# Kernel tuning notes

Measured on AMD Instinct MI355X. Metric: run time of the kernel, lower is better.

## Reference

```python
import jax, jax.numpy as jnp
import numpy as np

B, H, T, IN_DIM, OUT_DIM = 4096, 256, 128, 7, 3

def _u(key, shape, fan_in):
    s = 1.0 / np.sqrt(fan_in)
    return jax.random.uniform(key, shape, jnp.float32, -s, s)

def setup_inputs() -> dict:
    key = jax.random.key(0)
    ks = jax.random.split(key, 12)
    return {
        "metadata": jax.random.normal(ks[0], (B, IN_DIM), jnp.float32),
        "target_seq_len": T,
        # encoder_fc: Linear(7, H) -> ReLU -> Linear(H, 2H) -> ReLU
        "W1": _u(ks[1], (H, IN_DIM), IN_DIM), "b1": _u(ks[2], (H,), IN_DIM),
        "W2": _u(ks[3], (2 * H, H), H),       "b2": _u(ks[4], (2 * H,), H),
        # decoder LSTM (single layer, torch gate order i,f,g,o)
        "Wih": _u(ks[5], (4 * H, OUT_DIM), H), "Whh": _u(ks[6], (4 * H, H), H),
        "bih": _u(ks[7], (4 * H,), H),         "bhh": _u(ks[8], (4 * H,), H),
        # fc_out: Linear(H, H//2) -> ReLU -> Linear(H//2, 3)
        "Wo1": _u(ks[9], (H // 2, H), H),      "bo1": _u(ks[10], (H // 2,), H),
        "Wo2": _u(ks[11], (OUT_DIM, H // 2), H // 2),
        "bo2": jnp.zeros((OUT_DIM,), jnp.float32),
    }

def reference(metadata, target_seq_len, W1, b1, W2, b2,
              Wih, Whh, bih, bhh, Wo1, bo1, Wo2, bo2):
    hid = Whh.shape[1]
    # encoder MLP -> [B, 2H]; split into initial (h0, c0)
    enc = jax.nn.relu(metadata @ W1.T + b1)
    enc = jax.nn.relu(enc @ W2.T + b2)
    h0, c0 = enc[:, :hid], enc[:, hid:]
    x0 = metadata[:, :3]  # first decoder input = start position

    def step(carry, _):
        h, c, x = carry
        gates = x @ Wih.T + bih + h @ Whh.T + bhh  # [B, 4H]
        i, f, g, o = jnp.split(gates, 4, axis=-1)
        c = jax.nn.sigmoid(f) * c + jax.nn.sigmoid(i) * jnp.tanh(g)
        h = jax.nn.sigmoid(o) * jnp.tanh(c)
        y = jax.nn.relu(h @ Wo1.T + bo1) @ Wo2.T + bo2  # [B, 3]
        return (h, c, y), y

    _, ys = jax.lax.scan(step, (h0, c0, x0), None, length=target_seq_len)
    return jnp.transpose(ys, (1, 0, 2))  # [B, T, 3]
```

## Files before the change

### kernel.cpp

```cpp
#include <hip/hip_runtime.h>

typedef __bf16 bf16_t;
typedef bf16_t bf16x8 __attribute__((ext_vector_type(8)));
typedef float  f32x4  __attribute__((ext_vector_type(4)));

#define MFMA16(A, B, C) __builtin_amdgcn_mfma_f32_16x16x32_bf16((A), (B), (C), 0, 0, 0)

static constexpr int KEXT   = 288;
static constexpr int HS     = 296;
static constexpr int GS     = 264;
static constexpr int TSTEPS = 128;
static constexpr int TILE_B = 16;

static constexpr int WALL_OFF = 0;
static constexpr int W2E_OFF  = 1152 * 288;
static constexpr int WO2E_OFF = W2E_OFF + 512 * 288;
static constexpr int WS_ELEMS = WO2E_OFF + 16 * 128;

__global__ __launch_bounds__(256) void prep_kernel(
    const float* __restrict__ W2,  const float* __restrict__ b2,
    const float* __restrict__ Wih, const float* __restrict__ Whh,
    const float* __restrict__ bih, const float* __restrict__ bhh,
    const float* __restrict__ Wo1, const float* __restrict__ bo1,
    const float* __restrict__ Wo2, bf16_t* __restrict__ ws)
{
    int idx = blockIdx.x * 256 + threadIdx.x;
    if (idx < 1152 * 288) {
        int r = idx / 288, k = idx - r * 288;
        float v = 0.f;
        if (r < 1024) {
            if (k < 256)       v = Whh[r * 256 + k];
            else if (k < 259)  v = Wih[r * 3 + (k - 256)];
            else if (k == 259) v = bih[r] + bhh[r];
        } else {
            int q = r - 1024;
            if (k < 256)       v = Wo1[q * 256 + k];
            else if (k == 259) v = bo1[q];
        }
        ws[WALL_OFF + idx] = (bf16_t)v;
    } else if (idx < W2E_OFF + 512 * 288) {
        int j = idx - W2E_OFF;
        int u = j / 288, k = j - u * 288;
        float v = 0.f;
        if (k < 256)       v = W2[u * 256 + k];
        else if (k == 259) v = b2[u];
        ws[idx] = (bf16_t)v;
    } else if (idx < WS_ELEMS) {
        int j = idx - WO2E_OFF;
        int d = j >> 7, q = j & 127;
        ws[idx] = (bf16_t)((d < 3) ? Wo2[d * 128 + q] : 0.f);
    }
}

__device__ __forceinline__ float rcp_f(float x) {
    float r; asm("v_rcp_f32 %0, %1" : "=v"(r) : "v"(x)); return r;
}
__device__ __forceinline__ float sigm(float x) { return rcp_f(1.f + __expf(-x)); }
__device__ __forceinline__ float tanh_f(float x) {
    float e = __expf(2.f * x);
    return 1.f - 2.f * rcp_f(e + 1.f);
}
__device__ __forceinline__ unsigned pk2(float a, float b) {
    union { bf16_t h[2]; unsigned u; } x;
    x.h[0] = (bf16_t)a; x.h[1] = (bf16_t)b; return x.u;
}

__device__ __forceinline__ void bar_lds() {
    asm volatile("s_waitcnt lgkmcnt(0)" ::: "memory");
    __builtin_amdgcn_s_barrier();
}

__global__ __launch_bounds__(512, 2) void lstm_main(
    const float* __restrict__ meta, const float* __restrict__ W1,
    const float* __restrict__ b1,   const float* __restrict__ bo2,
    const bf16_t* __restrict__ ws,  float* __restrict__ out)
{
    __shared__ __align__(16) bf16_t hx[2][TILE_B][HS];
    __shared__ __align__(16) bf16_t wg[256][GS];
    __shared__ __align__(16) bf16_t wo2l[16][136];
    __shared__ __align__(16) bf16_t zbuf[TILE_B][136];

    const int tid  = threadIdx.x;
    const int wv   = tid >> 6;
    const int lane = tid & 63;
    const int l15  = lane & 15;
    const int quad = lane >> 4;
    const int gb   = blockIdx.x * TILE_B;

    const bf16_t* wall = ws + WALL_OFF;
    const bf16_t* w2e  = ws + W2E_OFF;
    const bf16_t* wo2e = ws + WO2E_OFF;
    const f32x4 zero4 = {0.f, 0.f, 0.f, 0.f};

    if (tid < 32) {
        int buf = tid >> 4, b = tid & 15;
        for (int c2 = 256; c2 < HS; ++c2)
            hx[buf][b][c2] = (bf16_t)((c2 == 259) ? 1.f : 0.f);
    }
    {
        int b = tid & 15, j0 = (tid >> 4) * 8;
        float m[7];
        #pragma unroll
        for (int k = 0; k < 7; ++k) m[k] = meta[(size_t)(gb + b) * 7 + k];
        #pragma unroll
        for (int jj = 0; jj < 8; ++jj) {
            int jd = j0 + jj;
            float acc = b1[jd];
            #pragma unroll
            for (int k = 0; k < 7; ++k) acc += W1[jd * 7 + k] * m[k];
            hx[1][b][jd] = (bf16_t)fmaxf(acc, 0.f);
        }
    }
    __syncthreads();

    float* cbuf = (float*)&wg[0][0];
    {
        f32x4 e[4] = {zero4, zero4, zero4, zero4};
        #pragma unroll
        for (int kk = 0; kk < 9; ++kk) {
            int ko = 32 * kk + 8 * quad;
            bf16x8 bf = *(const bf16x8*)&hx[1][l15][ko];
            #pragma unroll
            for (int m = 0; m < 4; ++m) {
                bf16x8 aa = *(const bf16x8*)&w2e[(size_t)(64 * wv + 16 * m + l15) * KEXT + ko];
                e[m] = MFMA16(aa, bf, e[m]);
            }
        }
        #pragma unroll
        for (int m = 0; m < 4; ++m) {
            int row = 64 * wv + 16 * m + 4 * quad;
            if (row < 256) {
                *(unsigned*)&hx[0][l15][row]     = pk2(fmaxf(e[m][0], 0.f), fmaxf(e[m][1], 0.f));
                *(unsigned*)&hx[0][l15][row + 2] = pk2(fmaxf(e[m][2], 0.f), fmaxf(e[m][3], 0.f));
            } else {
                int d = row - 256;
                #pragma unroll
                for (int r = 0; r < 4; ++r)
                    cbuf[(size_t)(d + r) * 17 + l15] = fmaxf(e[m][r], 0.f);
            }
        }
    }
    __syncthreads();

    f32x4 c[2];
    #pragma unroll
    for (int half = 0; half < 2; ++half)
        #pragma unroll
        for (int r = 0; r < 4; ++r)
            c[half][r] = cbuf[(size_t)(32 * wv + 16 * half + 4 * quad + r) * 17 + l15];
    __syncthreads();

    #pragma unroll
    for (int i = 0; i < 17; ++i) {
        int idx = tid + 512 * i;
        if (idx < 256 * 33) {
            int r = idx / 33, c8 = idx - r * 33;
            *(bf16x8*)&wg[r][8 * c8] = *(const bf16x8*)&wall[(size_t)(512 + r) * KEXT + 8 * c8];
        }
    }
    #pragma unroll
    for (int i = 0; i < 4; ++i) {
        int idx = tid + 512 * i;
        int r = idx >> 7, cc = idx & 127;
        wo2l[r][cc] = wo2e[r * 128 + cc];
    }

    bf16x8 af[2][2][9];
    #pragma unroll
    for (int g = 0; g < 2; ++g)
        #pragma unroll
        for (int h = 0; h < 2; ++h)
            #pragma unroll
            for (int kk = 0; kk < 9; ++kk)
                af[g][h][kk] = *(const bf16x8*)&wall[(size_t)(256 * g + 32 * wv + 16 * h + l15) * KEXT
                                                     + 32 * kk + 8 * quad];

    const bf16_t* obase = wall + (size_t)(768  + 32 * wv + l15) * KEXT + 8 * quad;
    const bf16_t* wbase = wall + (size_t)(1024 + 16 * wv + l15) * KEXT + 8 * quad;

    const float bo2v0 = bo2[0], bo2v1 = bo2[1], bo2v2 = bo2[2];

    bf16x8 ob[3][2];
    #pragma unroll
    for (int s = 0; s < 3; ++s)
        #pragma unroll
        for (int h = 0; h < 2; ++h)
            ob[s][h] = *(const bf16x8*)(obase + (size_t)(16 * h) * KEXT + 32 * s);

    bf16x8 xf;
    #pragma unroll
    for (int j = 0; j < 8; ++j) xf[j] = (bf16_t)0.f;
    if (quad == 0) {
        xf[0] = (bf16_t)meta[(size_t)(gb + l15) * 7 + 0];
        xf[1] = (bf16_t)meta[(size_t)(gb + l15) * 7 + 1];
        xf[2] = (bf16_t)meta[(size_t)(gb + l15) * 7 + 2];
        xf[3] = (bf16_t)1.f;
    }

    __syncthreads();

    for (int i = 0; i < TSTEPS; ++i) {
        const bf16_t (*cur)[HS] = hx[i & 1];
        bf16_t (*nxt)[HS]       = hx[(i + 1) & 1];

        f32x4 acc[4][2];
        #pragma unroll
        for (int g = 0; g < 4; ++g) { acc[g][0] = zero4; acc[g][1] = zero4; }

        #pragma unroll
        for (int kk = 0; kk < 9; ++kk) {
            int ko = 32 * kk + 8 * quad;
            bf16x8 bf = (kk < 8) ? *(const bf16x8*)&cur[l15][ko] : xf;
            #pragma unroll
            for (int h = 0; h < 2; ++h) {
                bf16x8 ag = *(const bf16x8*)&wg[32 * wv + 16 * h + l15][ko];
                acc[0][h] = MFMA16(af[0][h][kk], bf, acc[0][h]);
                acc[1][h] = MFMA16(af[1][h][kk], bf, acc[1][h]);
                acc[2][h] = MFMA16(ag,            bf, acc[2][h]);
                acc[3][h] = MFMA16(ob[kk % 3][h], bf, acc[3][h]);
            }
            #pragma unroll
            for (int h = 0; h < 2; ++h)
                ob[kk % 3][h] = *(const bf16x8*)(obase + (size_t)(16 * h) * KEXT
                                                 + 32 * ((kk + 3) % 9));
        }

        bf16x8 wrf[9];
        {
            float hh[4];
            #pragma unroll
            for (int r = 0; r < 4; ++r) {
                float iv = acc[0][0][r], fv = acc[1][0][r];
                float gv = acc[2][0][r], ov = acc[3][0][r];
                float cc = sigm(fv) * c[0][r] + sigm(iv) * tanh_f(gv);
                c[0][r] = cc;
                hh[r] = sigm(ov) * tanh_f(cc);
            }
            int dim = 32 * wv + 4 * quad;
            *(unsigned*)&nxt[l15][dim]     = pk2(hh[0], hh[1]);
            *(unsigned*)&nxt[l15][dim + 2] = pk2(hh[2], hh[3]);
        }
        #pragma unroll
        for (int s = 0; s < 5; ++s) wrf[s] = *(const bf16x8*)(wbase + 32 * s);
        {
            float hh[4];
            #pragma unroll
            for (int r = 0; r < 4; ++r) {
                float iv = acc[0][1][r], fv = acc[1][1][r];
                float gv = acc[2][1][r], ov = acc[3][1][r];
                float cc = sigm(fv) * c[1][r] + sigm(iv) * tanh_f(gv);
                c[1][r] = cc;
                hh[r] = sigm(ov) * tanh_f(cc);
            }
            int dim = 32 * wv + 16 + 4 * quad;
            *(unsigned*)&nxt[l15][dim]     = pk2(hh[0], hh[1]);
            *(unsigned*)&nxt[l15][dim + 2] = pk2(hh[2], hh[3]);
        }
        #pragma unroll
        for (int s = 5; s < 9; ++s) wrf[s] = *(const bf16x8*)(wbase + 32 * s);
        bar_lds();

        {
            bf16x8 zb[3];
            #pragma unroll
            for (int s = 0; s < 3; ++s)
                zb[s] = *(const bf16x8*)&nxt[l15][32 * s + 8 * quad];
            f32x4 za0 = zero4, za1 = zero4;
            #pragma unroll
            for (int kk = 0; kk < 9; ++kk) {
                if (kk & 1) za1 = MFMA16(wrf[kk], zb[kk % 3], za1);
                else        za0 = MFMA16(wrf[kk], zb[kk % 3], za0);
                if (kk + 3 <= 8)
                    zb[kk % 3] = *(const bf16x8*)&nxt[l15][32 * (kk + 3) + 8 * quad];
            }
            f32x4 za = za0 + za1;
            int zd = 16 * wv + 4 * quad;
            *(unsigned*)&zbuf[l15][zd]     = pk2(fmaxf(za[0], 0.f), fmaxf(za[1], 0.f));
            *(unsigned*)&zbuf[l15][zd + 2] = pk2(fmaxf(za[2], 0.f), fmaxf(za[3], 0.f));
        }
        bar_lds();

        {
            bf16x8 w2b[4], zbb[4];
            #pragma unroll
            for (int kk = 0; kk < 4; ++kk) {
                int ko = 32 * kk + 8 * quad;
                w2b[kk] = *(const bf16x8*)&wo2l[l15][ko];
                zbb[kk] = *(const bf16x8*)&zbuf[l15][ko];
            }
            f32x4 ya0 = zero4, ya1 = zero4;
            #pragma unroll
            for (int kk = 0; kk < 4; ++kk) {
                if (kk & 2) ya1 = MFMA16(w2b[kk], zbb[kk], ya1);
                else        ya0 = MFMA16(w2b[kk], zbb[kk], ya0);
            }
            f32x4 yv = ya0 + ya1;
            float y0 = yv[0] + bo2v0, y1 = yv[1] + bo2v1, y2 = yv[2] + bo2v2;
            if (wv == (i & 7) && quad == 0) {
                float* op = out + ((size_t)(gb + l15) * TSTEPS + i) * 3;
                op[0] = y0; op[1] = y1; op[2] = y2;
            }
            if (quad == 0) {
                xf[0] = (bf16_t)y0; xf[1] = (bf16_t)y1; xf[2] = (bf16_t)y2; xf[3] = (bf16_t)1.f;
            }
        }
    }
}

extern "C" void kernel_launch(void* const* d_in, const int* in_sizes, int n_in,
                              void* d_out, int out_size, void* d_ws, size_t ws_size,
                              hipStream_t stream)
{
    const float* meta = (const float*)d_in[0];
    const float* W1   = (const float*)d_in[2];
    const float* b1   = (const float*)d_in[3];
    const float* W2   = (const float*)d_in[4];
    const float* b2   = (const float*)d_in[5];
    const float* Wih  = (const float*)d_in[6];
    const float* Whh  = (const float*)d_in[7];
    const float* bih  = (const float*)d_in[8];
    const float* bhh  = (const float*)d_in[9];
    const float* Wo1  = (const float*)d_in[10];
    const float* bo1  = (const float*)d_in[11];
    const float* Wo2  = (const float*)d_in[12];
    const float* bo2  = (const float*)d_in[13];
    bf16_t* ws  = (bf16_t*)d_ws;
    float*  out = (float*)d_out;

    prep_kernel<<<dim3((WS_ELEMS + 255) / 256), dim3(256), 0, stream>>>(
        W2, b2, Wih, Whh, bih, bhh, Wo1, bo1, Wo2, ws);
    lstm_main<<<dim3(4096 / TILE_B), dim3(512), 0, stream>>>(
        meta, W1, b1, bo2, ws, out);
}
```

Before: 630.8 us.

## Software-pipeline LSTM step to overlap hidden-state gate MFMAs with output head

Peels the first gate computation out of the time loop and rotates the loop body. Each iteration now computes the fc_out head on the current h, then issues the h@Whh gate MFMAs (k-blocks 0..7) before the y-dependent input block. Only the final x block of the gate GEMM waits on y, so most gate work sits off the y->x critical path and can overlap the output-head latency. The cost is more complex double-buffer indexing and extra live registers for the gate accumulators during the head computation. The peeled extra step computes one LSTM update beyond the last output, which wastes a small amount of work.

Measured after the change: 616.8 us. 2.2% less time.

```diff
diff --git a/kernel.cpp b/kernel.cpp
--- a/kernel.cpp
+++ b/kernel.cpp
@@ -197,12 +197,11 @@
         xf[3] = (bf16_t)1.f;
     }
 
+    bf16x8 wrf[9];
+
     __syncthreads();
 
-    for (int i = 0; i < TSTEPS; ++i) {
-        const bf16_t (*cur)[HS] = hx[i & 1];
-        bf16_t (*nxt)[HS]       = hx[(i + 1) & 1];
-
+    {
         f32x4 acc[4][2];
         #pragma unroll
         for (int g = 0; g < 4; ++g) { acc[g][0] = zero4; acc[g][1] = zero4; }
@@ -210,7 +209,7 @@
         #pragma unroll
         for (int kk = 0; kk < 9; ++kk) {
             int ko = 32 * kk + 8 * quad;
-            bf16x8 bf = (kk < 8) ? *(const bf16x8*)&cur[l15][ko] : xf;
+            bf16x8 bf = (kk < 8) ? *(const bf16x8*)&hx[0][l15][ko] : xf;
             #pragma unroll
             for (int h = 0; h < 2; ++h) {
                 bf16x8 ag = *(const bf16x8*)&wg[32 * wv + 16 * h + l15][ko];
@@ -224,8 +223,6 @@
                 ob[kk % 3][h] = *(const bf16x8*)(obase + (size_t)(16 * h) * KEXT
                                                  + 32 * ((kk + 3) % 9));
         }
-
-        bf16x8 wrf[9];
         {
             float hh[4];
             #pragma unroll
@@ -237,8 +234,8 @@
                 hh[r] = sigm(ov) * tanh_f(cc);
             }
             int dim = 32 * wv + 4 * quad;
-            *(unsigned*)&nxt[l15][dim]     = pk2(hh[0], hh[1]);
-            *(unsigned*)&nxt[l15][dim + 2] = pk2(hh[2], hh[3]);
+            *(unsigned*)&hx[1][l15][dim]     = pk2(hh[0], hh[1]);
+            *(unsigned*)&hx[1][l15][dim + 2] = pk2(hh[2], hh[3]);
         }
         #pragma unroll
         for (int s = 0; s < 5; ++s) wrf[s] = *(const bf16x8*)(wbase + 32 * s);
@@ -253,25 +250,30 @@
                 hh[r] = sigm(ov) * tanh_f(cc);
             }
             int dim = 32 * wv + 16 + 4 * quad;
-            *(unsigned*)&nxt[l15][dim]     = pk2(hh[0], hh[1]);
-            *(unsigned*)&nxt[l15][dim + 2] = pk2(hh[2], hh[3]);
+            *(unsigned*)&hx[1][l15][dim]     = pk2(hh[0], hh[1]);
+            *(unsigned*)&hx[1][l15][dim + 2] = pk2(hh[2], hh[3]);
         }
         #pragma unroll
         for (int s = 5; s < 9; ++s) wrf[s] = *(const bf16x8*)(wbase + 32 * s);
-        bar_lds();
+    }
+    bar_lds();
+
+    for (int i = 0; i < TSTEPS; ++i) {
+        const bf16_t (*cur)[HS] = hx[(i + 1) & 1];
+        bf16_t (*nxt)[HS]       = hx[i & 1];
 
         {
             bf16x8 zb[3];
             #pragma unroll
             for (int s = 0; s < 3; ++s)
-                zb[s] = *(const bf16x8*)&nxt[l15][32 * s + 8 * quad];
+                zb[s] = *(const bf16x8*)&cur[l15][32 * s + 8 * quad];
             f32x4 za0 = zero4, za1 = zero4;
             #pragma unroll
             for (int kk = 0; kk < 9; ++kk) {
                 if (kk & 1) za1 = MFMA16(wrf[kk], zb[kk % 3], za1);
                 else        za0 = MFMA16(wrf[kk], zb[kk % 3], za0);
                 if (kk + 3 <= 8)
-                    zb[kk % 3] = *(const bf16x8*)&nxt[l15][32 * (kk + 3) + 8 * quad];
+                    zb[kk % 3] = *(const bf16x8*)&cur[l15][32 * (kk + 3) + 8 * quad];
             }
             f32x4 za = za0 + za1;
             int zd = 16 * wv + 4 * quad;
@@ -280,19 +282,37 @@
         }
         bar_lds();
 
-        {
-            bf16x8 w2b[4], zbb[4];
+        f32x4 acc[4][2];
+        #pragma unroll
+        for (int g = 0; g < 4; ++g) { acc[g][0] = zero4; acc[g][1] = zero4; }
+
+        #pragma unroll
+        for (int kk = 0; kk < 8; ++kk) {
+            int ko = 32 * kk + 8 * quad;
+            bf16x8 bf = *(const bf16x8*)&cur[l15][ko];
+            #pragma unroll
+            for (int h = 0; h < 2; ++h) {
+                bf16x8 ag = *(const bf16x8*)&wg[32 * wv + 16 * h + l15][ko];
+                acc[0][h] = MFMA16(af[0][h][kk], bf, acc[0][h]);
+                acc[1][h] = MFMA16(af[1][h][kk], bf, acc[1][h]);
+                acc[2][h] = MFMA16(ag,            bf, acc[2][h]);
+                acc[3][h] = MFMA16(ob[kk % 3][h], bf, acc[3][h]);
+            }
+            #pragma unroll
+            for (int h = 0; h < 2; ++h)
+                ob[kk % 3][h] = *(const bf16x8*)(obase + (size_t)(16 * h) * KEXT
+                                                 + 32 * ((kk + 3) % 9));
+        }
+
+        {
+            f32x4 ya0 = zero4, ya1 = zero4;
             #pragma unroll
             for (int kk = 0; kk < 4; ++kk) {
                 int ko = 32 * kk + 8 * quad;
-                w2b[kk] = *(const bf16x8*)&wo2l[l15][ko];
-                zbb[kk] = *(const bf16x8*)&zbuf[l15][ko];
-            }
-            f32x4 ya0 = zero4, ya1 = zero4;
-            #pragma unroll
-            for (int kk = 0; kk < 4; ++kk) {
-                if (kk & 2) ya1 = MFMA16(w2b[kk], zbb[kk], ya1);
-                else        ya0 = MFMA16(w2b[kk], zbb[kk], ya0);
+                bf16x8 w2 = *(const bf16x8*)&wo2l[l15][ko];
+                bf16x8 zz = *(const bf16x8*)&zbuf[l15][ko];
+                if (kk & 2) ya1 = MFMA16(w2, zz, ya1);
+                else        ya0 = MFMA16(w2, zz, ya0);
             }
             f32x4 yv = ya0 + ya1;
             float y0 = yv[0] + bo2v0, y1 = yv[1] + bo2v1, y2 = yv[2] + bo2v2;
@@ -304,6 +324,54 @@
                 xf[0] = (bf16_t)y0; xf[1] = (bf16_t)y1; xf[2] = (bf16_t)y2; xf[3] = (bf16_t)1.f;
             }
         }
+
+        {
+            #pragma unroll
+            for (int h = 0; h < 2; ++h) {
+                bf16x8 ag8 = *(const bf16x8*)&wg[32 * wv + 16 * h + l15][256 + 8 * quad];
+                acc[0][h] = MFMA16(af[0][h][8], xf, acc[0][h]);
+                acc[1][h] = MFMA16(af[1][h][8], xf, acc[1][h]);
+                acc[2][h] = MFMA16(ag8,         xf, acc[2][h]);
+                acc[3][h] = MFMA16(ob[2][h],    xf, acc[3][h]);
+            }
+            #pragma unroll
+            for (int h = 0; h < 2; ++h)
+                ob[2][h] = *(const bf16x8*)(obase + (size_t)(16 * h) * KEXT + 32 * 2);
+        }
+
+        {
+            float hh[4];
+            #pragma unroll
+            for (int r = 0; r < 4; ++r) {
+                float iv = acc[0][0][r], fv = acc[1][0][r];
+                float gv = acc[2][0][r], ov = acc[3][0][r];
+                float cc = sigm(fv) * c[0][r] + sigm(iv) * tanh_f(gv);
+                c[0][r] = cc;
+                hh[r] = sigm(ov) * tanh_f(cc);
+            }
+            int dim = 32 * wv + 4 * quad;
+            *(unsigned*)&nxt[l15][dim]     = pk2(hh[0], hh[1]);
+            *(unsigned*)&nxt[l15][dim + 2] = pk2(hh[2], hh[3]);
+        }
+        #pragma unroll
+        for (int s = 0; s < 5; ++s) wrf[s] = *(const bf16x8*)(wbase + 32 * s);
+        {
+            float hh[4];
+            #pragma unroll
+            for (int r = 0; r < 4; ++r) {
+                float iv = acc[0][1][r], fv = acc[1][1][r];
+                float gv = acc[2][1][r], ov = acc[3][1][r];
+                float cc = sigm(fv) * c[1][r] + sigm(iv) * tanh_f(gv);
+                c[1][r] = cc;
+                hh[r] = sigm(ov) * tanh_f(cc);
+            }
+            int dim = 32 * wv + 16 + 4 * quad;
+            *(unsigned*)&nxt[l15][dim]     = pk2(hh[0], hh[1]);
+            *(unsigned*)&nxt[l15][dim + 2] = pk2(hh[2], hh[3]);
+        }
+        #pragma unroll
+        for (int s = 5; s < 9; ++s) wrf[s] = *(const bf16x8*)(wbase + 32 * s);
+        bar_lds();
     }
 }
 
```
